# Kernel tuning notes

Hardware: AMD Instinct MI355X
Metric: run time of the kernel (lower is better)

## Reference

```python
import jax, jax.numpy as jnp
import numpy as np

B, P, E, H = 2, 4096, 512, 8
D = E // H
EPS = 1e-5


def _layernorm2d(x, g, b):
    # LayerNorm over last two dims (patches, embed) jointly, per torch nn.LayerNorm([P, E])
    mu = jnp.mean(x, axis=(-2, -1), keepdims=True)
    var = jnp.mean(jnp.square(x - mu), axis=(-2, -1), keepdims=True)
    return (x - mu) * jax.lax.rsqrt(var + EPS) * g + b


def setup_inputs() -> dict:
    key = jax.random.key(0)
    ks = jax.random.split(key, 4)
    s_in = 1.0 / np.sqrt(E)
    s_hid = 1.0 / np.sqrt(3 * E)
    return {
        "x": jax.random.normal(ks[0], (B, P, E), dtype=jnp.float32),
        "g1": jnp.ones((P, E), jnp.float32),
        "b1": jnp.zeros((P, E), jnp.float32),
        "W1": jax.random.normal(ks[1], (3 * E, E), jnp.float32) * s_in,
        "g2": jnp.ones((P, E), jnp.float32),
        "b2": jnp.zeros((P, E), jnp.float32),
        "Wa": jax.random.normal(ks[2], (3 * E, E), jnp.float32) * s_in,
        "ba": jnp.zeros((3 * E,), jnp.float32),
        "Wb": jax.random.normal(ks[3], (E, 3 * E), jnp.float32) * s_hid,
        "bb": jnp.zeros((E,), jnp.float32),
    }


def reference(x, g1, b1, W1, g2, b2, Wa, ba, Wb, bb):
    # --- attention branch ---
    h = _layernorm2d(x, g1, b1)                      # [B,P,E]
    qkv = h @ W1.T                                   # [B,P,3E]
    qkv = qkv.reshape(B, P, 3, H, D).transpose(2, 0, 3, 1, 4)  # [3,B,H,P,D]
    q, k, v = qkv[0], qkv[1], qkv[2]
    scale = 1.0 / jnp.sqrt(jnp.float32(D))
    dp = jnp.einsum("bhqd,bhkd->bhqk", q, k) * scale  # [B,H,P,P]
    # NOTE: softmax over axis -2 (the query axis), as in the original code
    dp = jax.nn.softmax(dp, axis=-2)
    wv = jnp.einsum("bhqk,bhkd->bhqd", dp, v)        # [B,H,P,D]
    wv = wv.transpose(0, 2, 1, 3).reshape(B, P, E)   # [B,P,E]
    out1 = x + wv
    # --- MLP branch ---
    h2 = _layernorm2d(out1, g2, b2)
    h2 = jax.nn.gelu(h2 @ Wa.T + ba, approximate=False)
    h2 = jax.nn.gelu(h2 @ Wb.T + bb, approximate=False)
    return h2 + out1
```

## Files before the change

kernel.cpp:

```cpp
#include <hip/hip_runtime.h>
#include <math.h>

typedef __bf16 bf16x8 __attribute__((ext_vector_type(8)));
typedef __bf16 bf16x4 __attribute__((ext_vector_type(4)));
typedef float f32x4 __attribute__((ext_vector_type(4)));
typedef unsigned short u16;
typedef unsigned int u32;

__device__ __forceinline__ void gl_lds16(const void* g, void* l) {
  __builtin_amdgcn_global_load_lds(
      (const __attribute__((address_space(1))) void*)g,
      (__attribute__((address_space(3))) void*)l, 16, 0, 0);
}

__device__ __forceinline__ u16 f2bf(float x) {
  union { float f; u32 u; } v; v.f = x;
  u32 r = v.u + 0x7FFFu + ((v.u >> 16) & 1u);
  return (u16)(r >> 16);
}

__device__ __forceinline__ u32 pack_bf2(float a, float b) {
  union { float f; u32 u; } ua, ub; ua.f = a; ub.f = b;
  return ((ua.u + 0x8000u) >> 16) | ((ub.u + 0x8000u) & 0xFFFF0000u);
}

__device__ __forceinline__ float expfast(float x) {
#if __has_builtin(__builtin_amdgcn_exp2f)
  return __builtin_amdgcn_exp2f(x);
#else
  return exp2f(x);
#endif
}

__device__ __forceinline__ float gelu_f(float v) {
  return 0.5f * v * (1.0f + erff(v * 0.7071067811865475f));
}

__global__ void cast_lnred(const float* __restrict__ s0, const float* __restrict__ s1,
                           const float* __restrict__ s2, u16* __restrict__ d0,
                           u16* __restrict__ d1, u16* __restrict__ d2,
                           const float* __restrict__ x, float2* __restrict__ part) {
  int blk = blockIdx.x;
  if (blk < 2304) {
    const float* s; u16* d;
    if (blk < 768)       { s = s0; d = d0; }
    else if (blk < 1536) { s = s1; d = d1; blk -= 768; }
    else                 { s = s2; d = d2; blk -= 1536; }
    int i = blk * 256 + threadIdx.x;
    float4 v = ((const float4*)s)[i];
    uint2 o;
    o.x = (u32)f2bf(v.x) | ((u32)f2bf(v.y) << 16);
    o.y = (u32)f2bf(v.z) | ((u32)f2bf(v.w) << 16);
    ((uint2*)d)[i] = o;
    return;
  }
  blk -= 2304;
  int b = blk >> 7, ib = blk & 127;
  const float4* p = (const float4*)(x + (size_t)b * 2097152 + (size_t)ib * 16384);
  float s = 0.f, q = 0.f;
  #pragma unroll
  for (int i = 0; i < 16; i++) {
    float4 v = p[i * 256 + threadIdx.x];
    s += v.x + v.y + v.z + v.w;
    q += v.x * v.x + v.y * v.y + v.z * v.z + v.w * v.w;
  }
  #pragma unroll
  for (int off = 32; off; off >>= 1) { s += __shfl_down(s, off, 64); q += __shfl_down(q, off, 64); }
  __shared__ float ls[4], lq[4];
  int w = threadIdx.x >> 6;
  if ((threadIdx.x & 63) == 0) { ls[w] = s; lq[w] = q; }
  __syncthreads();
  if (threadIdx.x == 0)
    part[b * 128 + ib] =
        make_float2(ls[0] + ls[1] + ls[2] + ls[3], lq[0] + lq[1] + lq[2] + lq[3]);
}

__global__ void ln_reduce(const float* __restrict__ src, float2* __restrict__ part) {
  int b = blockIdx.y;
  const float4* p = (const float4*)(src + (size_t)b * 2097152 + (size_t)blockIdx.x * 16384);
  float s = 0.f, q = 0.f;
  #pragma unroll
  for (int i = 0; i < 16; i++) {
    float4 v = p[i * 256 + threadIdx.x];
    s += v.x + v.y + v.z + v.w;
    q += v.x * v.x + v.y * v.y + v.z * v.z + v.w * v.w;
  }
  #pragma unroll
  for (int off = 32; off; off >>= 1) { s += __shfl_down(s, off, 64); q += __shfl_down(q, off, 64); }
  __shared__ float ls[4], lq[4];
  int w = threadIdx.x >> 6;
  if ((threadIdx.x & 63) == 0) { ls[w] = s; lq[w] = q; }
  __syncthreads();
  if (threadIdx.x == 0)
    part[b * 128 + blockIdx.x] =
        make_float2(ls[0] + ls[1] + ls[2] + ls[3], lq[0] + lq[1] + lq[2] + lq[3]);
}

__global__ void ln_apply(const float* __restrict__ src, const float* __restrict__ g,
                         const float* __restrict__ bta, const float2* __restrict__ part,
                         u16* __restrict__ dst) {
  int i = blockIdx.x * 256 + threadIdx.x;
  int b = i >= 524288;
  int lane = threadIdx.x & 63;
  float2 a = part[b * 128 + lane], c2 = part[b * 128 + 64 + lane];
  float s = a.x + c2.x, q = a.y + c2.y;
  #pragma unroll
  for (int off = 32; off; off >>= 1) { s += __shfl_down(s, off, 64); q += __shfl_down(q, off, 64); }
  s = __shfl(s, 0, 64); q = __shfl(q, 0, 64);
  const float inv = 1.0f / 2097152.0f;
  float mu = s * inv;
  float rsig = rsqrtf(q * inv - mu * mu + 1e-5f);
  int r = i - b * 524288;
  float4 v = ((const float4*)src)[i];
  float4 gv = ((const float4*)g)[r];
  float4 bv = ((const float4*)bta)[r];
  float h0 = (v.x - mu) * rsig * gv.x + bv.x;
  float h1 = (v.y - mu) * rsig * gv.y + bv.y;
  float h2 = (v.z - mu) * rsig * gv.z + bv.z;
  float h3 = (v.w - mu) * rsig * gv.w + bv.w;
  uint2 o;
  o.x = (u32)f2bf(h0) | ((u32)f2bf(h1) << 16);
  o.y = (u32)f2bf(h2) | ((u32)f2bf(h3) << 16);
  ((uint2*)dst)[i] = o;
}

template <int MODE>
__global__ __launch_bounds__(256, 2)
void gemm_bt(const u16* __restrict__ A, const u16* __restrict__ Bm,
             const float* __restrict__ bias, const float* __restrict__ res,
             float* __restrict__ outf, u16* __restrict__ outb,
             int M, int N, int K) {
  __shared__ u16 As[128 * 32], Bs[128 * 32];
  const int tid = threadIdx.x;
  const int m0 = blockIdx.y * 128, n0 = blockIdx.x * 128;
  const int lane = tid & 63, w = tid >> 6;
  const int wm = (w >> 1) * 64, wn = (w & 1) * 64;
  const int c = lane & 15, quad = lane >> 4;
  const int arow = tid >> 2, acol = (tid & 3) * 8;

  const u16* gA = A + (size_t)(m0 + arow) * K + acol;
  const u16* gB = Bm + (size_t)(n0 + arow) * K + acol;
  u16* lA = As + tid * 8;
  u16* lB = Bs + tid * 8;

  f32x4 acc[4][4] = {};
  for (int kt = 0; kt < K; kt += 32) {
    gl_lds16(gA, lA);
    gl_lds16(gA + (size_t)64 * K, lA + 64 * 32);
    gl_lds16(gB, lB);
    gl_lds16(gB + (size_t)64 * K, lB + 64 * 32);
    gA += 32; gB += 32;
    __syncthreads();
    bf16x8 af[4], bf[4];
    #pragma unroll
    for (int i = 0; i < 4; i++) {
      af[i] = *(const bf16x8*)&As[(wm + i * 16 + c) * 32 + quad * 8];
      bf[i] = *(const bf16x8*)&Bs[(wn + i * 16 + c) * 32 + quad * 8];
    }
    #pragma unroll
    for (int i = 0; i < 4; i++)
      #pragma unroll
      for (int j = 0; j < 4; j++)
        acc[i][j] = __builtin_amdgcn_mfma_f32_16x16x32_bf16(af[i], bf[j], acc[i][j], 0, 0, 0);
    __syncthreads();
  }
  #pragma unroll
  for (int i = 0; i < 4; i++) {
    const int row0 = m0 + wm + i * 16 + quad * 4;
    #pragma unroll
    for (int j = 0; j < 4; j++) {
      const int col = n0 + wn + j * 16 + c;
      #pragma unroll
      for (int r = 0; r < 4; r++) {
        float v = acc[i][j][r];
        size_t oi = (size_t)(row0 + r) * N + col;
        if (MODE == 0 && col < 512) v *= 0.1803368801111204f;
        if (MODE == 1 || MODE == 2) v = gelu_f(v + bias[col]);
        if (MODE == 2) outf[oi] = v + res[oi];
        else           outb[oi] = f2bf(v);
      }
    }
  }
}

__global__ __launch_bounds__(256, 4)
void attn_pass1(const u16* __restrict__ qkv, float* __restrict__ rlpart) {
  __shared__ u16 Qs[2][2 * 128 * 32];
  const int tid = threadIdx.x;
  const int bh = blockIdx.y, b = bh >> 3, h = bh & 7;
  const int k0 = blockIdx.x * 128;
  const int lane = tid & 63, w = tid >> 6;
  const int wn = w * 32;
  const int c = lane & 15, quad = lane >> 4;
  const int arow = tid >> 2, acol = (tid & 3) * 8;

  bf16x8 bk[2][2];
  {
    const u16* Kg = qkv + ((size_t)(b * 4096 + k0 + wn + c)) * 1536 + 512 + h * 64 + quad * 8;
    #pragma unroll
    for (int j = 0; j < 2; j++)
      #pragma unroll
      for (int ks = 0; ks < 2; ks++)
        bk[j][ks] = *(const bf16x8*)(Kg + (size_t)j * 16 * 1536 + ks * 32);
  }
  const u16* Qg = qkv + ((size_t)(b * 4096 + blockIdx.z * 2048)) * 1536 + h * 64;

  #define STAGE_Q(t)                                                              \
    {                                                                             \
      u16* dst = Qs[(t) & 1];                                                     \
      const u16* src = Qg + (size_t)((t) * 128) * 1536;                           \
      _Pragma("unroll")                                                           \
      for (int ks = 0; ks < 2; ks++)                                              \
        _Pragma("unroll")                                                         \
        for (int rr = 0; rr < 128; rr += 64)                                      \
          gl_lds16(src + (size_t)(rr + arow) * 1536 + ks * 32 + acol,             \
                   dst + ks * 4096 + (rr + arow) * 32 + acol);                    \
    }

  STAGE_Q(0);
  float s0 = 0.f, s1 = 0.f;
  for (int t = 0; t < 16; t++) {
    __syncthreads();
    if (t + 1 < 16) STAGE_Q(t + 1);
    const u16* buf = Qs[t & 1];
    #pragma unroll
    for (int i = 0; i < 8; i++) {
      bf16x8 a0 = *(const bf16x8*)&buf[(i * 16 + c) * 32 + quad * 8];
      bf16x8 a1 = *(const bf16x8*)&buf[4096 + (i * 16 + c) * 32 + quad * 8];
      f32x4 acc0 = {}, acc1 = {};
      acc0 = __builtin_amdgcn_mfma_f32_16x16x32_bf16(a0, bk[0][0], acc0, 0, 0, 0);
      acc0 = __builtin_amdgcn_mfma_f32_16x16x32_bf16(a1, bk[0][1], acc0, 0, 0, 0);
      acc1 = __builtin_amdgcn_mfma_f32_16x16x32_bf16(a0, bk[1][0], acc1, 0, 0, 0);
      acc1 = __builtin_amdgcn_mfma_f32_16x16x32_bf16(a1, bk[1][1], acc1, 0, 0, 0);
      #pragma unroll
      for (int r = 0; r < 4; r++) {
        s0 += expfast(acc0[r]);
        s1 += expfast(acc1[r]);
      }
    }
  }
  #undef STAGE_Q
  s0 += __shfl_xor(s0, 16, 64); s0 += __shfl_xor(s0, 32, 64);
  s1 += __shfl_xor(s1, 16, 64); s1 += __shfl_xor(s1, 32, 64);
  if (quad == 0) {
    float* rp = rlpart + ((size_t)blockIdx.z * 16 + bh) * 4096 + k0 + wn;
    rp[c] = s0;
    rp[16 + c] = s1;
  }
}

__global__ void vtrans(const u16* __restrict__ qkv, const float* __restrict__ rlpart,
                       u16* __restrict__ vt) {
  __shared__ u16 t[64 * 66];
  __shared__ float rls[64];
  int bh = blockIdx.y, p0 = blockIdx.x * 64;
  int b = bh >> 3, h = bh & 7;
  const u16* src = qkv + ((size_t)(b * 4096 + p0)) * 1536 + 1024 + h * 64;
  int tid = threadIdx.x;
  if (tid < 64) {
    size_t idx = (size_t)bh * 4096 + p0 + tid;
    rls[tid] = 1.0f / (rlpart[idx] + rlpart[65536 + idx]);
  }
  __syncthreads();
  #pragma unroll
  for (int j = 0; j < 16; j++) {
    int idx = j * 256 + tid;
    int p = idx >> 6, d = idx & 63;
    union { float f; u32 u; } uv;
    uv.u = ((u32)src[(size_t)p * 1536 + d]) << 16;
    t[d * 66 + p] = f2bf(uv.f * rls[p]);
  }
  __syncthreads();
  u16* dst = vt + (size_t)bh * 262144 + (size_t)blockIdx.x * 4096;
  #pragma unroll
  for (int j = 0; j < 16; j++) {
    int idx = j * 256 + tid;
    int d = idx >> 6, p = idx & 63;
    dst[d * 64 + ((((p >> 3) & 7) ^ (d & 7)) << 3) + (p & 7)] = t[d * 66 + p];
  }
}

__global__ __launch_bounds__(256, 2)
void attn_pass2(const u16* __restrict__ qkv, const u16* __restrict__ vt,
                const float* __restrict__ x, float* __restrict__ out1) {
  __shared__ u16 Ks[2][2][2048];
  __shared__ u16 Vs[2][4096];
  __shared__ u16 Ps[128][64];
  const int tid = threadIdx.x;
  const int bh = blockIdx.y, b = bh >> 3, h = bh & 7;
  const int q0 = blockIdx.x * 128;
  const int lane = tid & 63, w = tid >> 6;
  const int wq = w * 32;
  const int c = lane & 15, quad = lane >> 4;

  bf16x8 bq[2][2];
  {
    const u16* Qg = qkv + ((size_t)(b * 4096 + q0 + wq + c)) * 1536 + h * 64 + quad * 8;
    #pragma unroll
    for (int j = 0; j < 2; j++)
      #pragma unroll
      for (int ks = 0; ks < 2; ks++)
        bq[j][ks] = *(const bf16x8*)(Qg + (size_t)j * 16 * 1536 + ks * 32);
  }
  const u16* Kg = qkv + ((size_t)b * 4096) * 1536 + 512 + h * 64;
  const u16* Vg = vt + (size_t)bh * 262144;

  #define STAGE_KV(t)                                                             \
    {                                                                             \
      const int buf_ = (t) & 1;                                                   \
      const int krow_ = (t) * 64 + (tid >> 2);                                    \
      _Pragma("unroll")                                                           \
      for (int ks = 0; ks < 2; ks++)                                              \
        gl_lds16(Kg + (size_t)krow_ * 1536 + ks * 32 + (tid & 3) * 8,             \
                 &Ks[buf_][ks][tid * 8]);                                         \
      gl_lds16(Vg + (t) * 4096 + tid * 8, &Vs[buf_][tid * 8]);                    \
      gl_lds16(Vg + (t) * 4096 + 2048 + tid * 8, &Vs[buf_][2048 + tid * 8]);      \
    }

  STAGE_KV(0);
  f32x4 oacc[2][4] = {};
  for (int t = 0; t < 64; t++) {
    __syncthreads();
    if (t + 1 < 64) STAGE_KV(t + 1);
    const int buf = t & 1;

    f32x4 sacc[4][2] = {};
    #pragma unroll
    for (int i = 0; i < 4; i++) {
      bf16x8 af0 = *(const bf16x8*)&Ks[buf][0][(i * 16 + c) * 32 + quad * 8];
      bf16x8 af1 = *(const bf16x8*)&Ks[buf][1][(i * 16 + c) * 32 + quad * 8];
      #pragma unroll
      for (int j = 0; j < 2; j++) {
        sacc[i][j] = __builtin_amdgcn_mfma_f32_16x16x32_bf16(af0, bq[j][0], sacc[i][j], 0, 0, 0);
        sacc[i][j] = __builtin_amdgcn_mfma_f32_16x16x32_bf16(af1, bq[j][1], sacc[i][j], 0, 0, 0);
      }
    }
    #pragma unroll
    for (int i = 0; i < 4; i++) {
      const int blk = i * 2 + (quad >> 1);
      #pragma unroll
      for (int j = 0; j < 2; j++) {
        const int qloc = wq + j * 16 + c;
        u16* pp = &Ps[qloc][((blk ^ (qloc & 7)) << 3) + ((quad & 1) << 2)];
        uint2 pk;
        pk.x = pack_bf2(expfast(sacc[i][j][0]), expfast(sacc[i][j][1]));
        pk.y = pack_bf2(expfast(sacc[i][j][2]), expfast(sacc[i][j][3]));
        *(uint2*)pp = pk;
      }
    }
    #pragma unroll
    for (int kg = 0; kg < 2; kg++) {
      bf16x8 pf[2], vf[4];
      #pragma unroll
      for (int j = 0; j < 2; j++) {
        const int qloc = wq + j * 16 + c;
        const int blk = kg * 4 + quad;
        pf[j] = *(const bf16x8*)&Ps[qloc][(blk ^ (qloc & 7)) << 3];
      }
      #pragma unroll
      for (int dt = 0; dt < 4; dt++) {
        const int d = dt * 16 + c;
        const int vblk = kg * 4 + quad;
        vf[dt] = *(const bf16x8*)&Vs[buf][d * 64 + ((vblk ^ (d & 7)) << 3)];
      }
      #pragma unroll
      for (int j = 0; j < 2; j++)
        #pragma unroll
        for (int dt = 0; dt < 4; dt++)
          oacc[j][dt] = __builtin_amdgcn_mfma_f32_16x16x32_bf16(pf[j], vf[dt], oacc[j][dt], 0, 0, 0);
    }
  }
  #undef STAGE_KV
  #pragma unroll
  for (int j = 0; j < 2; j++)
    #pragma unroll
    for (int dt = 0; dt < 4; dt++)
      #pragma unroll
      for (int r = 0; r < 4; r++) {
        const int q = q0 + wq + j * 16 + quad * 4 + r;
        const int d = dt * 16 + c;
        size_t oi = ((size_t)(b * 4096 + q)) * 512 + h * 64 + d;
        out1[oi] = x[oi] + oacc[j][dt][r];
      }
}

extern "C" void kernel_launch(void* const* d_in, const int* in_sizes, int n_in,
                              void* d_out, int out_size, void* d_ws, size_t ws_size,
                              hipStream_t stream) {
  const float* x  = (const float*)d_in[0];
  const float* g1 = (const float*)d_in[1];
  const float* b1 = (const float*)d_in[2];
  const float* W1 = (const float*)d_in[3];
  const float* g2 = (const float*)d_in[4];
  const float* b2 = (const float*)d_in[5];
  const float* Wa = (const float*)d_in[6];
  const float* ba = (const float*)d_in[7];
  const float* Wb = (const float*)d_in[8];
  const float* bb = (const float*)d_in[9];
  float* out = (float*)d_out;

  char* ws = (char*)d_ws;
  u16* w1b   = (u16*)(ws);
  u16* wab   = (u16*)(ws + 1572864);
  u16* wbb   = (u16*)(ws + 3145728);
  u16* h1    = (u16*)(ws + 4718592);
  u16* qkv   = (u16*)(ws + 13107200);
  u16* vt    = (u16*)(ws + 38273024);
  u16* h2    = (u16*)(ws + 46661632);
  u16* mid   = (u16*)(ws + 55050240);
  float* o1  = (float*)(ws + 80478208);
  float2* part  = (float2*)(ws + 97255424);
  float* rlpart = (float*)(ws + 55050240);

  cast_lnred<<<2560, 256, 0, stream>>>(W1, Wa, Wb, w1b, wab, wbb, x, part);
  ln_apply<<<4096, 256, 0, stream>>>(x, g1, b1, part, h1);

  gemm_bt<0><<<dim3(12, 64), 256, 0, stream>>>(h1, w1b, nullptr, nullptr, nullptr, qkv,
                                               8192, 1536, 512);
  attn_pass1<<<dim3(32, 16, 2), 256, 0, stream>>>(qkv, rlpart);
  vtrans<<<dim3(64, 16), 256, 0, stream>>>(qkv, rlpart, vt);
  attn_pass2<<<dim3(32, 16), 256, 0, stream>>>(qkv, vt, x, o1);

  ln_reduce<<<dim3(128, 2), 256, 0, stream>>>(o1, part);
  ln_apply<<<4096, 256, 0, stream>>>(o1, g2, b2, part, h2);

  gemm_bt<1><<<dim3(12, 64), 256, 0, stream>>>(h2, wab, ba, nullptr, nullptr, mid,
                                               8192, 1536, 512);
  gemm_bt<2><<<dim3(4, 64), 256, 0, stream>>>(mid, wbb, bb, o1, out, nullptr,
                                              8192, 512, 1536);
}
```

Measured before the change: 367.3 us.

## Split attention pass2 over key halves, keep P in registers, fuse combine into LN reduce

Result: no change. 363.8 us (-1.0%).

```diff
diff --git a/kernel.cpp b/kernel.cpp
--- a/kernel.cpp
+++ b/kernel.cpp
@@ -3,7 +3,9 @@
 
 typedef __bf16 bf16x8 __attribute__((ext_vector_type(8)));
 typedef __bf16 bf16x4 __attribute__((ext_vector_type(4)));
+typedef short s16x4 __attribute__((ext_vector_type(4)));
 typedef float f32x4 __attribute__((ext_vector_type(4)));
+typedef unsigned int u32x2 __attribute__((ext_vector_type(2)));
 typedef unsigned short u16;
 typedef unsigned int u32;
 
@@ -17,6 +19,13 @@
   union { float f; u32 u; } v; v.f = x;
   u32 r = v.u + 0x7FFFu + ((v.u >> 16) & 1u);
   return (u16)(r >> 16);
+}
+
+__device__ __forceinline__ float bflo(u32 u) {
+  union { float f; u32 v; } t; t.v = u << 16; return t.f;
+}
+__device__ __forceinline__ float bfhi(u32 u) {
+  union { float f; u32 v; } t; t.v = u & 0xFFFF0000u; return t.f;
 }
 
 __device__ __forceinline__ u32 pack_bf2(float a, float b) {
@@ -29,6 +38,15 @@
   return __builtin_amdgcn_exp2f(x);
 #else
   return exp2f(x);
+#endif
+}
+
+__device__ __forceinline__ f32x4 mfma16(bf16x4 a, bf16x4 b, f32x4 c) {
+#if __has_builtin(__builtin_amdgcn_mfma_f32_16x16x16_bf16)
+  return __builtin_amdgcn_mfma_f32_16x16x16_bf16(a, b, c, 0, 0, 0);
+#else
+  return __builtin_amdgcn_mfma_f32_16x16x16bf16_1k(
+      __builtin_bit_cast(s16x4, a), __builtin_bit_cast(s16x4, b), c, 0, 0, 0);
 #endif
 }
 
@@ -75,13 +93,24 @@
         make_float2(ls[0] + ls[1] + ls[2] + ls[3], lq[0] + lq[1] + lq[2] + lq[3]);
 }
 
-__global__ void ln_reduce(const float* __restrict__ src, float2* __restrict__ part) {
-  int b = blockIdx.y;
-  const float4* p = (const float4*)(src + (size_t)b * 2097152 + (size_t)blockIdx.x * 16384);
+__global__ void comb_lnred(const float* __restrict__ x, const u16* __restrict__ opart,
+                           float* __restrict__ o1, float2* __restrict__ part) {
+  int blk = blockIdx.x;
+  size_t base = (size_t)blk * 4096;
+  const uint2* oa = (const uint2*)opart;
+  const uint2* ob = (const uint2*)(opart + 4194304);
   float s = 0.f, q = 0.f;
   #pragma unroll
   for (int i = 0; i < 16; i++) {
-    float4 v = p[i * 256 + threadIdx.x];
+    size_t idx = base + i * 256 + threadIdx.x;
+    float4 v = ((const float4*)x)[idx];
+    uint2 a = oa[idx];
+    uint2 c = ob[idx];
+    v.x += bflo(a.x) + bflo(c.x);
+    v.y += bfhi(a.x) + bfhi(c.x);
+    v.z += bflo(a.y) + bflo(c.y);
+    v.w += bfhi(a.y) + bfhi(c.y);
+    ((float4*)o1)[idx] = v;
     s += v.x + v.y + v.z + v.w;
     q += v.x * v.x + v.y * v.y + v.z * v.z + v.w * v.w;
   }
@@ -92,8 +121,7 @@
   if ((threadIdx.x & 63) == 0) { ls[w] = s; lq[w] = q; }
   __syncthreads();
   if (threadIdx.x == 0)
-    part[b * 128 + blockIdx.x] =
-        make_float2(ls[0] + ls[1] + ls[2] + ls[3], lq[0] + lq[1] + lq[2] + lq[3]);
+    part[blk] = make_float2(ls[0] + ls[1] + ls[2] + ls[3], lq[0] + lq[1] + lq[2] + lq[3]);
 }
 
 __global__ void ln_apply(const float* __restrict__ src, const float* __restrict__ g,
@@ -280,15 +308,15 @@
   }
 }
 
-__global__ __launch_bounds__(256, 2)
+__global__ __launch_bounds__(256, 4)
 void attn_pass2(const u16* __restrict__ qkv, const u16* __restrict__ vt,
-                const float* __restrict__ x, float* __restrict__ out1) {
+                u16* __restrict__ opart) {
   __shared__ u16 Ks[2][2][2048];
   __shared__ u16 Vs[2][4096];
-  __shared__ u16 Ps[128][64];
   const int tid = threadIdx.x;
   const int bh = blockIdx.y, b = bh >> 3, h = bh & 7;
   const int q0 = blockIdx.x * 128;
+  const int kh = blockIdx.z;
   const int lane = tid & 63, w = tid >> 6;
   const int wq = w * 32;
   const int c = lane & 15, quad = lane >> 4;
@@ -302,8 +330,8 @@
       for (int ks = 0; ks < 2; ks++)
         bq[j][ks] = *(const bf16x8*)(Qg + (size_t)j * 16 * 1536 + ks * 32);
   }
-  const u16* Kg = qkv + ((size_t)b * 4096) * 1536 + 512 + h * 64;
-  const u16* Vg = vt + (size_t)bh * 262144;
+  const u16* Kg = qkv + ((size_t)(b * 4096 + kh * 2048)) * 1536 + 512 + h * 64;
+  const u16* Vg = vt + (size_t)bh * 262144 + (size_t)kh * 131072;
 
   #define STAGE_KV(t)                                                             \
     {                                                                             \
@@ -319,9 +347,9 @@
 
   STAGE_KV(0);
   f32x4 oacc[2][4] = {};
-  for (int t = 0; t < 64; t++) {
+  for (int t = 0; t < 32; t++) {
     __syncthreads();
-    if (t + 1 < 64) STAGE_KV(t + 1);
+    if (t + 1 < 32) STAGE_KV(t + 1);
     const int buf = t & 1;
 
     f32x4 sacc[4][2] = {};
@@ -335,52 +363,39 @@
         sacc[i][j] = __builtin_amdgcn_mfma_f32_16x16x32_bf16(af1, bq[j][1], sacc[i][j], 0, 0, 0);
       }
     }
-    #pragma unroll
-    for (int i = 0; i < 4; i++) {
-      const int blk = i * 2 + (quad >> 1);
+    bf16x4 pa[4][2];
+    #pragma unroll
+    for (int i = 0; i < 4; i++)
       #pragma unroll
       for (int j = 0; j < 2; j++) {
-        const int qloc = wq + j * 16 + c;
-        u16* pp = &Ps[qloc][((blk ^ (qloc & 7)) << 3) + ((quad & 1) << 2)];
-        uint2 pk;
+        u32x2 pk;
         pk.x = pack_bf2(expfast(sacc[i][j][0]), expfast(sacc[i][j][1]));
         pk.y = pack_bf2(expfast(sacc[i][j][2]), expfast(sacc[i][j][3]));
-        *(uint2*)pp = pk;
-      }
-    }
-    #pragma unroll
-    for (int kg = 0; kg < 2; kg++) {
-      bf16x8 pf[2], vf[4];
-      #pragma unroll
-      for (int j = 0; j < 2; j++) {
-        const int qloc = wq + j * 16 + c;
-        const int blk = kg * 4 + quad;
-        pf[j] = *(const bf16x8*)&Ps[qloc][(blk ^ (qloc & 7)) << 3];
-      }
-      #pragma unroll
-      for (int dt = 0; dt < 4; dt++) {
-        const int d = dt * 16 + c;
-        const int vblk = kg * 4 + quad;
-        vf[dt] = *(const bf16x8*)&Vs[buf][d * 64 + ((vblk ^ (d & 7)) << 3)];
-      }
-      #pragma unroll
-      for (int j = 0; j < 2; j++)
-        #pragma unroll
-        for (int dt = 0; dt < 4; dt++)
-          oacc[j][dt] = __builtin_amdgcn_mfma_f32_16x16x32_bf16(pf[j], vf[dt], oacc[j][dt], 0, 0, 0);
+        pa[i][j] = __builtin_bit_cast(bf16x4, pk);
+      }
+    #pragma unroll
+    for (int kc = 0; kc < 4; kc++) {
+      const int kb = 2 * kc + (quad >> 1);
+      #pragma unroll
+      for (int j2 = 0; j2 < 4; j2++) {
+        const int d = j2 * 16 + c;
+        bf16x4 vf = *(const bf16x4*)&Vs[buf][d * 64 + ((kb ^ (d & 7)) << 3) + 4 * (quad & 1)];
+        oacc[0][j2] = mfma16(pa[kc][0], vf, oacc[0][j2]);
+        oacc[1][j2] = mfma16(pa[kc][1], vf, oacc[1][j2]);
+      }
     }
   }
   #undef STAGE_KV
-  #pragma unroll
-  for (int j = 0; j < 2; j++)
-    #pragma unroll
-    for (int dt = 0; dt < 4; dt++)
+  u16* op = opart + (size_t)kh * 4194304;
+  #pragma unroll
+  for (int i2 = 0; i2 < 2; i2++)
+    #pragma unroll
+    for (int j2 = 0; j2 < 4; j2++)
       #pragma unroll
       for (int r = 0; r < 4; r++) {
-        const int q = q0 + wq + j * 16 + quad * 4 + r;
-        const int d = dt * 16 + c;
-        size_t oi = ((size_t)(b * 4096 + q)) * 512 + h * 64 + d;
-        out1[oi] = x[oi] + oacc[j][dt][r];
+        const int q = q0 + wq + i2 * 16 + quad * 4 + r;
+        const int d = j2 * 16 + c;
+        op[((size_t)(b * 4096 + q)) * 512 + h * 64 + d] = f2bf(oacc[i2][j2][r]);
       }
 }
 
@@ -411,6 +426,7 @@
   float* o1  = (float*)(ws + 80478208);
   float2* part  = (float2*)(ws + 97255424);
   float* rlpart = (float*)(ws + 55050240);
+  u16* opart    = (u16*)(ws + 55050240);
 
   cast_lnred<<<2560, 256, 0, stream>>>(W1, Wa, Wb, w1b, wab, wbb, x, part);
   ln_apply<<<4096, 256, 0, stream>>>(x, g1, b1, part, h1);
@@ -419,9 +435,9 @@
                                                8192, 1536, 512);
   attn_pass1<<<dim3(32, 16, 2), 256, 0, stream>>>(qkv, rlpart);
   vtrans<<<dim3(64, 16), 256, 0, stream>>>(qkv, rlpart, vt);
-  attn_pass2<<<dim3(32, 16), 256, 0, stream>>>(qkv, vt, x, o1);
-
-  ln_reduce<<<dim3(128, 2), 256, 0, stream>>>(o1, part);
+  attn_pass2<<<dim3(32, 16, 2), 256, 0, stream>>>(qkv, vt, opart);
+
+  comb_lnred<<<256, 256, 0, stream>>>(x, opart, o1, part);
   ln_apply<<<4096, 256, 0, stream>>>(o1, g2, b2, part, h2);
 
   gemm_bt<1><<<dim3(12, 64), 256, 0, stream>>>(h2, wab, ba, nullptr, nullptr, mid,
```
